# Performance work log

Hardware: AMD Instinct MI355X
Metric: run time of the kernel (lower is better)

## Reference

```python
import jax, jax.numpy as jnp
import numpy as np

P = 32    # cardinality (number of parallel paths)
C = 256   # block input/output channels
D = 4     # bottleneck width per path
EPS = 1e-3  # Keras BatchNormalization default epsilon


def setup_inputs() -> dict:
    key = jax.random.key(0)
    ks = jax.random.split(key, 24)
    def nrm(k, shape, s=0.05):
        return jax.random.normal(k, shape, dtype=jnp.float32) * s
    inp = {}
    inp["x"] = jax.random.normal(ks[0], (8, 56, 56, C), dtype=jnp.float32)
    # conv weights/biases, stacked over the path axis P
    inp["W1"] = nrm(ks[1], (P, C, D))          # 1x1 conv C->4
    inp["B1"] = nrm(ks[2], (P, D))
    inp["W2"] = nrm(ks[3], (P, 3, 3, D, D))    # 3x3 conv 4->4 (HWIO)
    inp["B2"] = nrm(ks[4], (P, D))
    inp["W3"] = nrm(ks[5], (P, D, C))          # 1x1 conv 4->256
    inp["B3"] = nrm(ks[6], (P, C))
    # BatchNorm (inference): gamma, beta, moving mean, moving var per stage
    inp["G1"]  = 1.0 + nrm(ks[7], (P, D));  inp["Be1"] = nrm(ks[8], (P, D))
    inp["M1"]  = nrm(ks[9], (P, D));        inp["V1"]  = 1.0 + 0.1 * jax.random.uniform(ks[10], (P, D), dtype=jnp.float32)
    inp["G2"]  = 1.0 + nrm(ks[11], (P, D)); inp["Be2"] = nrm(ks[12], (P, D))
    inp["M2"]  = nrm(ks[13], (P, D));       inp["V2"]  = 1.0 + 0.1 * jax.random.uniform(ks[14], (P, D), dtype=jnp.float32)
    inp["G3"]  = 1.0 + nrm(ks[15], (P, C)); inp["Be3"] = nrm(ks[16], (P, C))
    inp["M3"]  = nrm(ks[17], (P, C));       inp["V3"]  = 1.0 + 0.1 * jax.random.uniform(ks[18], (P, C), dtype=jnp.float32)
    return inp


def _bn(x, g, b, m, v):
    # inference batch-norm: affine over channel axis
    return g * (x - m) * jax.lax.rsqrt(v + EPS) + b


def _path(x, w1, b1, g1, be1, m1, v1, w2, b2, g2, be2, m2, v2, w3, b3, g3, be3, m3, v3):
    h = jnp.einsum('nhwc,cd->nhwd', x, w1) + b1            # 1x1 conv C->D
    h = jax.nn.relu(_bn(h, g1, be1, m1, v1))
    h = jax.lax.conv_general_dilated(
        h, w2, window_strides=(1, 1), padding='SAME',
        dimension_numbers=('NHWC', 'HWIO', 'NHWC')) + b2   # 3x3 conv D->D
    h = jax.nn.relu(_bn(h, g2, be2, m2, v2))
    h = jnp.einsum('nhwd,dc->nhwc', h, w3) + b3            # 1x1 conv D->C
    h = jax.nn.relu(_bn(h, g3, be3, m3, v3))
    return h  # Dropout(0.2) is identity at inference


def reference(x, W1, B1, G1, Be1, M1, V1, W2, B2, G2, Be2, M2, V2, W3, B3, G3, Be3, M3, V3):
    # vmap over the 32 cardinality paths; x is shared (in_axes=None)
    paths = jax.vmap(_path, in_axes=(None,) + (0,) * 18)(
        x, W1, B1, G1, Be1, M1, V1, W2, B2, G2, Be2, M2, V2, W3, B3, G3, Be3, M3, V3)
    return jax.nn.relu(paths.sum(axis=0) + x)
```

## Files before the change

### kernel.cpp

```cpp
#include <hip/hip_runtime.h>

#define BATCH 8
#define HH 56
#define WW 56
#define NPOS (BATCH*HH*WW)
#define C 256
#define P 32
#define D 4
#define J 128
#define EPS 1e-3f

typedef __attribute__((ext_vector_type(8))) short bf16x8_t;
typedef __attribute__((ext_vector_type(4))) float f32x4_t;

__device__ __forceinline__ unsigned short f2bf(float f) {
    union { float f; unsigned int i; } v; v.f = f;
    unsigned int r = v.i + 0x7fffu + ((v.i >> 16) & 1u);
    return (unsigned short)(r >> 16);
}
__device__ __forceinline__ uint2 pack4_trunc(float4 v) {
    uint2 r;
    r.x = __builtin_amdgcn_perm(__float_as_uint(v.y), __float_as_uint(v.x), 0x07060302u);
    r.y = __builtin_amdgcn_perm(__float_as_uint(v.w), __float_as_uint(v.z), 0x07060302u);
    return r;
}

__global__ __launch_bounds__(256) void fold_params(
    const float* __restrict__ W1, const float* __restrict__ B1,
    const float* __restrict__ W2, const float* __restrict__ B2,
    const float* __restrict__ W3, const float* __restrict__ B3,
    const float* __restrict__ G1, const float* __restrict__ Be1,
    const float* __restrict__ M1, const float* __restrict__ V1,
    const float* __restrict__ G2, const float* __restrict__ Be2,
    const float* __restrict__ M2, const float* __restrict__ V2,
    const float* __restrict__ G3, const float* __restrict__ Be3,
    const float* __restrict__ M3, const float* __restrict__ V3,
    unsigned short* __restrict__ W1bf, float* __restrict__ b1f,
    float* __restrict__ w2q, float* __restrict__ b2t,
    unsigned short* __restrict__ WB)
{
    int idx = blockIdx.x * 256 + threadIdx.x;

    if (idx < C*J) {
        int j = idx >> 8, c = idx & 255;
        int p = j >> 2, d = j & 3;
        float s = G1[j] * rsqrtf(V1[j] + EPS);
        W1bf[idx] = f2bf(W1[(p*C + c)*D + d] * s);
        return;
    }
    idx -= C*J;
    if (idx < J) {
        float s = G1[idx] * rsqrtf(V1[idx] + EPS);
        b1f[idx] = B1[idx] * s + Be1[idx] - M1[idx] * s;
        return;
    }
    idx -= J;
    if (idx < 9*D*D*P) {
        int do_ = idx & 3, p = (idx >> 2) & 31;
        int r2 = idx >> 7, di = r2 & 3, k9 = r2 >> 2;
        int j = p*4 + do_;
        float s = G2[j] * rsqrtf(V2[j] + EPS);
        w2q[idx] = W2[((p*9 + k9)*4 + di)*4 + do_] * s;
        return;
    }
    idx -= 9*D*D*P;
    if (idx < J) {
        int do_ = idx >> 5, p = idx & 31;
        int j = p*4 + do_;
        float s = G2[j] * rsqrtf(V2[j] + EPS);
        b2t[idx] = B2[j] * s + Be2[j] - M2[j] * s;
        return;
    }
    idx -= J;
    if (idx < P*C*8) {
        int s8 = idx & 7;
        int c = (idx >> 3) & 255;
        int p = idx >> 11;
        float sc = G3[p*C + c] * rsqrtf(V3[p*C + c] + EPS);
        float v = 0.f;
        if (s8 < 4)       v = W3[(p*D + s8)*C + c] * sc;
        else if (s8 == 4) v = B3[p*C + c] * sc + Be3[p*C + c] - M3[p*C + c] * sc;
        WB[idx] = f2bf(v);
        return;
    }
}

__global__ __launch_bounds__(256) void fused12(
    const float* __restrict__ x, const unsigned short* __restrict__ W1bf,
    const float* __restrict__ b1f, const float* __restrict__ w2q,
    const float* __restrict__ b2t, unsigned short* __restrict__ h2)
{
    __shared__ unsigned short xs[64*256];
    __shared__ unsigned short h1L[64*132];
    __shared__ float w2s[4608];
    __shared__ float bs[128];
    __shared__ float b1s[128];

    const int tid = threadIdx.x;
    int bxx = blockIdx.x;
    const int xb = bxx % 7;  bxx /= 7;
    const int yb = bxx % 14; const int b = bxx / 14;
    const int wid = tid >> 6, l = tid & 63, l15 = l & 15, quad = l >> 4;
    const int j0w = wid * 32;

    union bu { uint4 u; bf16x8_t v; };
    bu aw[2][8];
#pragma unroll
    for (int jf = 0; jf < 2; ++jf) {
        int row = j0w + jf*16 + l15;
#pragma unroll
        for (int kc = 0; kc < 8; ++kc)
            aw[jf][kc].u = *(const uint4*)&W1bf[row*C + kc*32 + quad*8];
    }

    for (int i = tid; i < 4608; i += 256) w2s[i] = w2q[i];
    if (tid < 128) { bs[tid] = b2t[tid]; b1s[tid] = b1f[tid]; }

#pragma unroll
    for (int it = 0; it < 8; ++it) {
        int idx = it*256 + tid;
        int pos = idx >> 5, g = idx & 31;
        uint4 st; st.x = 0u; st.y = 0u; st.z = 0u; st.w = 0u;
        if (pos < 60) {
            int hy = pos / 10, hx = pos - hy*10;
            int gy = yb*4 + hy - 1, gx = xb*8 + hx - 1;
            if (gy >= 0 && gy < HH && gx >= 0 && gx < WW) {
                const float* xp = &x[(size_t)((b*HH + gy)*WW + gx) * C + g*8];
                float4 v0 = *(const float4*)xp;
                float4 v1 = *(const float4*)(xp + 4);
                uint2 p0 = pack4_trunc(v0), p1 = pack4_trunc(v1);
                st.x = p0.x; st.y = p0.y; st.z = p1.x; st.w = p1.y;
            }
        }
        *(uint4*)&xs[pos*256 + ((g ^ (pos & 7)) * 8)] = st;
    }
    __syncthreads();

#pragma unroll
    for (int mt = 0; mt < 4; ++mt) {
        const int row = mt*16 + l15;
        int hy = (row * 205) >> 11;
        int hx = row - hy*10;
        int gy = yb*4 + hy - 1, gx = xb*8 + hx - 1;
        unsigned mask = (row < 60 && gy >= 0 && gy < HH && gx >= 0 && gx < WW)
                        ? 0xFFFFFFFFu : 0u;
        f32x4_t acc0 = (f32x4_t){0.f,0.f,0.f,0.f};
        f32x4_t acc1 = (f32x4_t){0.f,0.f,0.f,0.f};
#pragma unroll
        for (int kc = 0; kc < 8; ++kc) {
            int g = (kc*4 + quad) ^ (row & 7);
            bf16x8_t bb = *(const bf16x8_t*)&xs[row*256 + g*8];
            acc0 = __builtin_amdgcn_mfma_f32_16x16x32_bf16(aw[0][kc].v, bb, acc0, 0, 0, 0);
            acc1 = __builtin_amdgcn_mfma_f32_16x16x32_bf16(aw[1][kc].v, bb, acc1, 0, 0, 0);
        }
#pragma unroll
        for (int jf = 0; jf < 2; ++jf) {
            const f32x4_t a = jf ? acc1 : acc0;
            int jb = j0w + jf*16 + quad*4;
            float4 bias = *(const float4*)&b1s[jb];
            float v0 = fmaxf(a[0] + bias.x, 0.f);
            float v1 = fmaxf(a[1] + bias.y, 0.f);
            float v2 = fmaxf(a[2] + bias.z, 0.f);
            float v3 = fmaxf(a[3] + bias.w, 0.f);
            uint2 o;
            o.x = ((unsigned int)f2bf(v0) | ((unsigned int)f2bf(v1) << 16)) & mask;
            o.y = ((unsigned int)f2bf(v2) | ((unsigned int)f2bf(v3) << 16)) & mask;
            *(uint2*)&h1L[row*132 + jb] = o;
        }
    }
    __syncthreads();

    const int p = tid & 31;
    const int slot = tid >> 5;
    float acc[4][4];
#pragma unroll
    for (int i = 0; i < 4; ++i) {
        acc[i][0] = bs[p]; acc[i][1] = bs[32+p];
        acc[i][2] = bs[64+p]; acc[i][3] = bs[96+p];
    }
#pragma unroll
    for (int ky = 0; ky < 3; ++ky) {
#pragma unroll
        for (int kx = 0; kx < 3; ++kx) {
            const float* wp = &w2s[(ky*3 + kx) * 512 + p*4];
            float4 w0 = *(const float4*)&wp[0];
            float4 w1 = *(const float4*)&wp[128];
            float4 w2v = *(const float4*)&wp[256];
            float4 w3v = *(const float4*)&wp[384];
#pragma unroll
            for (int i = 0; i < 4; ++i) {
                int nl = slot + i*8;
                int hp = ((nl >> 3) + ky)*10 + (nl & 7) + kx;
                uint2 hv = *(const uint2*)&h1L[hp*132 + p*4];
                float f0 = __uint_as_float(hv.x << 16);
                float f1 = __uint_as_float(hv.x & 0xffff0000u);
                float f2 = __uint_as_float(hv.y << 16);
                float f3 = __uint_as_float(hv.y & 0xffff0000u);
                acc[i][0] = fmaf(f0, w0.x, acc[i][0]);  acc[i][1] = fmaf(f0, w0.y, acc[i][1]);
                acc[i][2] = fmaf(f0, w0.z, acc[i][2]);  acc[i][3] = fmaf(f0, w0.w, acc[i][3]);
                acc[i][0] = fmaf(f1, w1.x, acc[i][0]);  acc[i][1] = fmaf(f1, w1.y, acc[i][1]);
                acc[i][2] = fmaf(f1, w1.z, acc[i][2]);  acc[i][3] = fmaf(f1, w1.w, acc[i][3]);
                acc[i][0] = fmaf(f2, w2v.x, acc[i][0]); acc[i][1] = fmaf(f2, w2v.y, acc[i][1]);
                acc[i][2] = fmaf(f2, w2v.z, acc[i][2]); acc[i][3] = fmaf(f2, w2v.w, acc[i][3]);
                acc[i][0] = fmaf(f3, w3v.x, acc[i][0]); acc[i][1] = fmaf(f3, w3v.y, acc[i][1]);
                acc[i][2] = fmaf(f3, w3v.z, acc[i][2]); acc[i][3] = fmaf(f3, w3v.w, acc[i][3]);
            }
        }
    }
#pragma unroll
    for (int i = 0; i < 4; ++i) {
        int nl = slot + i*8;
        int gy = yb*4 + (nl >> 3), gx = xb*8 + (nl & 7);
        uint2 o;
        o.x = (unsigned int)f2bf(fmaxf(acc[i][0], 0.f)) |
              ((unsigned int)f2bf(fmaxf(acc[i][1], 0.f)) << 16);
        o.y = (unsigned int)f2bf(fmaxf(acc[i][2], 0.f)) |
              ((unsigned int)f2bf(fmaxf(acc[i][3], 0.f)) << 16);
        int n = (b*HH + gy)*WW + gx;
        *(uint2*)&h2[(size_t)n * J + p*4] = o;
    }
}

#define S3_STRIDE 136
__global__ __launch_bounds__(256, 3) void stage3(
    const unsigned short* __restrict__ h2,
    const unsigned short* __restrict__ WB,
    const float* __restrict__ x, float* __restrict__ out)
{
    __shared__ unsigned short h2s[64 * S3_STRIDE];
    __shared__ unsigned short wbf[P * 64 * 8];
    __shared__ unsigned short zz[8];

    const int tid = threadIdx.x;
    const int bx = blockIdx.x;
    const int cchunk = bx & 3, nchunk = bx >> 2;
    const int wid = tid >> 6, l = tid & 63, l15 = l & 15, quad = l >> 4;
    const int cb = cchunk * 64;
    const int cl = wid*16 + l15;
    const int c = cb + cl;
    const int n0 = nchunk * 64;

#pragma unroll
    for (int it = 0; it < 4; ++it) {
        int idx = it*256 + tid;
        int row = idx >> 4, col = (idx & 15) * 8;
        uint4 v = *(const uint4*)&h2[(size_t)(n0 + row) * J + col];
        *(uint4*)&h2s[row * S3_STRIDE + col] = v;
    }
#pragma unroll
    for (int it = 0; it < 8; ++it) {
        int e = it*256 + tid;
        int p = e >> 6, ecl = e & 63;
        uint4 u = *(const uint4*)&WB[((size_t)(p*C + cb + ecl)) * 8];
        *(uint4*)&wbf[(p*64 + ecl) * 8] = u;
    }
    if (tid < 8) zz[tid] = 0;
    __syncthreads();

    const unsigned short* bp = (quad == 0) ? &wbf[cl*8] : &zz[0];
    const int pstep = (quad == 0) ? 512 : 0;

    const f32x4_t zero = (f32x4_t){0.f, 0.f, 0.f, 0.f};
    f32x4_t acc[4];
#pragma unroll
    for (int i = 0; i < 4; ++i) acc[i] = zero;
    const unsigned int one = 0x3f80u;

#pragma unroll
    for (int p = 0; p < P; p += 2) {
        union { uint4 u; bf16x8_t v; } B0, B1;
        B0.u = *(const uint4*)(bp + p*pstep);
        B1.u = *(const uint4*)(bp + (p+1)*pstep);
#pragma unroll
        for (int pass = 0; pass < 4; ++pass) {
            uint4 h8 = *(const uint4*)&h2s[(pass*16 + l15) * S3_STRIDE + p*4];
            union { unsigned int u[4]; bf16x8_t v; } A0, A1;
            A0.u[0] = h8.x; A0.u[1] = h8.y; A0.u[2] = one; A0.u[3] = 0u;
            A1.u[0] = h8.z; A1.u[1] = h8.w; A1.u[2] = one; A1.u[3] = 0u;
            f32x4_t z0 = __builtin_amdgcn_mfma_f32_16x16x32_bf16(A0.v, B0.v, zero, 0, 0, 0);
            f32x4_t z1 = __builtin_amdgcn_mfma_f32_16x16x32_bf16(A1.v, B1.v, zero, 0, 0, 0);
#pragma unroll
            for (int r = 0; r < 4; ++r)
                acc[pass][r] += fmaxf(z0[r], 0.f) + fmaxf(z1[r], 0.f);
        }
    }

#pragma unroll
    for (int pass = 0; pass < 4; ++pass) {
#pragma unroll
        for (int r = 0; r < 4; ++r) {
            int n = n0 + pass*16 + quad*4 + r;
            float v = acc[pass][r] + x[(size_t)n * C + c];
            out[(size_t)n * C + c] = fmaxf(v, 0.f);
        }
    }
}

extern "C" void kernel_launch(void* const* d_in, const int* in_sizes, int n_in,
                              void* d_out, int out_size, void* d_ws, size_t ws_size,
                              hipStream_t stream) {
    const float* x  = (const float*)d_in[0];
    const float* W1 = (const float*)d_in[1];
    const float* B1 = (const float*)d_in[2];
    const float* W2 = (const float*)d_in[3];
    const float* B2 = (const float*)d_in[4];
    const float* W3 = (const float*)d_in[5];
    const float* B3 = (const float*)d_in[6];
    const float* G1 = (const float*)d_in[7];
    const float* Be1= (const float*)d_in[8];
    const float* M1 = (const float*)d_in[9];
    const float* V1 = (const float*)d_in[10];
    const float* G2 = (const float*)d_in[11];
    const float* Be2= (const float*)d_in[12];
    const float* M2 = (const float*)d_in[13];
    const float* V2 = (const float*)d_in[14];
    const float* G3 = (const float*)d_in[15];
    const float* Be3= (const float*)d_in[16];
    const float* M3 = (const float*)d_in[17];
    const float* V3 = (const float*)d_in[18];

    char* wsb = (char*)d_ws;
    unsigned short* h2   = (unsigned short*)(wsb + 0);
    unsigned short* W1bf = (unsigned short*)(wsb + 6422528);
    unsigned short* WB   = (unsigned short*)(wsb + 6488064);
    float*          w2q  = (float*)(wsb + 6619136);
    float*          b1f  = (float*)(wsb + 6637568);
    float*          b2t  = (float*)(wsb + 6638080);

    const int fold_tasks = C*J + J + 9*D*D*P + J + P*C*8;
    fold_params<<<(fold_tasks + 255)/256, 256, 0, stream>>>(
        W1, B1, W2, B2, W3, B3, G1, Be1, M1, V1, G2, Be2, M2, V2,
        G3, Be3, M3, V3, W1bf, b1f, w2q, b2t, WB);

    fused12<<<8*14*7, 256, 0, stream>>>(x, W1bf, b1f, w2q, b2t, h2);
    stage3<<<(NPOS/64)*4, 256, 0, stream>>>(h2, WB, x, (float*)d_out);
}
```

Measured before the change: 160.1 us.

## Fuse stage3 expansion into fused12 kernel, keeping h2 tile in shared memory

```diff
diff --git a/kernel.cpp b/kernel.cpp
--- a/kernel.cpp
+++ b/kernel.cpp
@@ -9,6 +9,7 @@
 #define D 4
 #define J 128
 #define EPS 1e-3f
+#define H2S 136
 
 typedef __attribute__((ext_vector_type(8))) short bf16x8_t;
 typedef __attribute__((ext_vector_type(4))) float f32x4_t;
@@ -37,7 +38,7 @@
     const float* __restrict__ M3, const float* __restrict__ V3,
     unsigned short* __restrict__ W1bf, float* __restrict__ b1f,
     float* __restrict__ w2q, float* __restrict__ b2t,
-    unsigned short* __restrict__ WB)
+    unsigned short* __restrict__ WB, unsigned short* __restrict__ zb)
 {
     int idx = blockIdx.x * 256 + threadIdx.x;
 
@@ -83,18 +84,22 @@
         WB[idx] = f2bf(v);
         return;
     }
-}
-
-__global__ __launch_bounds__(256) void fused12(
+    idx -= P*C*8;
+    if (idx < 8) { zb[idx] = 0; return; }
+}
+
+__global__ __launch_bounds__(256) void fused_all(
     const float* __restrict__ x, const unsigned short* __restrict__ W1bf,
     const float* __restrict__ b1f, const float* __restrict__ w2q,
-    const float* __restrict__ b2t, unsigned short* __restrict__ h2)
+    const float* __restrict__ b2t, const unsigned short* __restrict__ WB,
+    const unsigned short* __restrict__ zb, float* __restrict__ out)
 {
     __shared__ unsigned short xs[64*256];
     __shared__ unsigned short h1L[64*132];
     __shared__ float w2s[4608];
     __shared__ float bs[128];
     __shared__ float b1s[128];
+    __shared__ unsigned short h2s[32*H2S];
 
     const int tid = threadIdx.x;
     int bxx = blockIdx.x;
@@ -210,88 +215,78 @@
 #pragma unroll
     for (int i = 0; i < 4; ++i) {
         int nl = slot + i*8;
-        int gy = yb*4 + (nl >> 3), gx = xb*8 + (nl & 7);
         uint2 o;
         o.x = (unsigned int)f2bf(fmaxf(acc[i][0], 0.f)) |
               ((unsigned int)f2bf(fmaxf(acc[i][1], 0.f)) << 16);
         o.y = (unsigned int)f2bf(fmaxf(acc[i][2], 0.f)) |
               ((unsigned int)f2bf(fmaxf(acc[i][3], 0.f)) << 16);
-        int n = (b*HH + gy)*WW + gx;
-        *(uint2*)&h2[(size_t)n * J + p*4] = o;
-    }
-}
-
-#define S3_STRIDE 136
-__global__ __launch_bounds__(256, 3) void stage3(
-    const unsigned short* __restrict__ h2,
-    const unsigned short* __restrict__ WB,
-    const float* __restrict__ x, float* __restrict__ out)
-{
-    __shared__ unsigned short h2s[64 * S3_STRIDE];
-    __shared__ unsigned short wbf[P * 64 * 8];
-    __shared__ unsigned short zz[8];
-
-    const int tid = threadIdx.x;
-    const int bx = blockIdx.x;
-    const int cchunk = bx & 3, nchunk = bx >> 2;
-    const int wid = tid >> 6, l = tid & 63, l15 = l & 15, quad = l >> 4;
-    const int cb = cchunk * 64;
-    const int cl = wid*16 + l15;
-    const int c = cb + cl;
-    const int n0 = nchunk * 64;
-
-#pragma unroll
-    for (int it = 0; it < 4; ++it) {
-        int idx = it*256 + tid;
-        int row = idx >> 4, col = (idx & 15) * 8;
-        uint4 v = *(const uint4*)&h2[(size_t)(n0 + row) * J + col];
-        *(uint4*)&h2s[row * S3_STRIDE + col] = v;
-    }
-#pragma unroll
-    for (int it = 0; it < 8; ++it) {
-        int e = it*256 + tid;
-        int p = e >> 6, ecl = e & 63;
-        uint4 u = *(const uint4*)&WB[((size_t)(p*C + cb + ecl)) * 8];
-        *(uint4*)&wbf[(p*64 + ecl) * 8] = u;
-    }
-    if (tid < 8) zz[tid] = 0;
+        *(uint2*)&h2s[nl*H2S + p*4] = o;
+    }
     __syncthreads();
 
-    const unsigned short* bp = (quad == 0) ? &wbf[cl*8] : &zz[0];
-    const int pstep = (quad == 0) ? 512 : 0;
+    const int cb = wid * 64;
+    const unsigned short* wbp;
+    int pstr, cstr;
+    if (quad == 0) {
+        wbp = &WB[((size_t)(cb + l15)) * 8];
+        pstr = C * 8;
+        cstr = 16 * 8;
+    } else {
+        wbp = zb;
+        pstr = 0; cstr = 0;
+    }
 
     const f32x4_t zero = (f32x4_t){0.f, 0.f, 0.f, 0.f};
-    f32x4_t acc[4];
-#pragma unroll
-    for (int i = 0; i < 4; ++i) acc[i] = zero;
+    f32x4_t dacc[2][4];
+#pragma unroll
+    for (int ps = 0; ps < 2; ++ps)
+#pragma unroll
+        for (int ct = 0; ct < 4; ++ct) dacc[ps][ct] = zero;
     const unsigned int one = 0x3f80u;
 
-#pragma unroll
-    for (int p = 0; p < P; p += 2) {
-        union { uint4 u; bf16x8_t v; } B0, B1;
-        B0.u = *(const uint4*)(bp + p*pstep);
-        B1.u = *(const uint4*)(bp + (p+1)*pstep);
-#pragma unroll
-        for (int pass = 0; pass < 4; ++pass) {
-            uint4 h8 = *(const uint4*)&h2s[(pass*16 + l15) * S3_STRIDE + p*4];
-            union { unsigned int u[4]; bf16x8_t v; } A0, A1;
-            A0.u[0] = h8.x; A0.u[1] = h8.y; A0.u[2] = one; A0.u[3] = 0u;
-            A1.u[0] = h8.z; A1.u[1] = h8.w; A1.u[2] = one; A1.u[3] = 0u;
-            f32x4_t z0 = __builtin_amdgcn_mfma_f32_16x16x32_bf16(A0.v, B0.v, zero, 0, 0, 0);
-            f32x4_t z1 = __builtin_amdgcn_mfma_f32_16x16x32_bf16(A1.v, B1.v, zero, 0, 0, 0);
-#pragma unroll
-            for (int r = 0; r < 4; ++r)
-                acc[pass][r] += fmaxf(z0[r], 0.f) + fmaxf(z1[r], 0.f);
-        }
-    }
-
-#pragma unroll
-    for (int pass = 0; pass < 4; ++pass) {
+#pragma unroll 2
+    for (int pp = 0; pp < 16; ++pp) {
+        uint4 h0 = *(const uint4*)&h2s[l15*H2S + pp*8];
+        uint4 h1 = *(const uint4*)&h2s[(16 + l15)*H2S + pp*8];
+        union au { unsigned int u[4]; bf16x8_t v; };
+        au A00, A01, A10, A11;
+        A00.u[0] = h0.x; A00.u[1] = h0.y; A00.u[2] = one; A00.u[3] = 0u;
+        A01.u[0] = h0.z; A01.u[1] = h0.w; A01.u[2] = one; A01.u[3] = 0u;
+        A10.u[0] = h1.x; A10.u[1] = h1.y; A10.u[2] = one; A10.u[3] = 0u;
+        A11.u[0] = h1.z; A11.u[1] = h1.w; A11.u[2] = one; A11.u[3] = 0u;
+        const unsigned short* pb0 = wbp + pp*2*pstr;
+        const unsigned short* pb1 = pb0 + pstr;
+#pragma unroll
+        for (int ct = 0; ct < 4; ++ct) {
+            union bu2 { uint4 u; bf16x8_t v; } B0, B1;
+            B0.u = *(const uint4*)(pb0 + ct*cstr);
+            B1.u = *(const uint4*)(pb1 + ct*cstr);
+            f32x4_t z00 = __builtin_amdgcn_mfma_f32_16x16x32_bf16(A00.v, B0.v, zero, 0, 0, 0);
+            f32x4_t z01 = __builtin_amdgcn_mfma_f32_16x16x32_bf16(A01.v, B1.v, zero, 0, 0, 0);
+            f32x4_t z10 = __builtin_amdgcn_mfma_f32_16x16x32_bf16(A10.v, B0.v, zero, 0, 0, 0);
+            f32x4_t z11 = __builtin_amdgcn_mfma_f32_16x16x32_bf16(A11.v, B1.v, zero, 0, 0, 0);
+#pragma unroll
+            for (int r = 0; r < 4; ++r) {
+                dacc[0][ct][r] += fmaxf(z00[r], 0.f) + fmaxf(z01[r], 0.f);
+                dacc[1][ct][r] += fmaxf(z10[r], 0.f) + fmaxf(z11[r], 0.f);
+            }
+        }
+    }
+
+#pragma unroll
+    for (int ps = 0; ps < 2; ++ps) {
 #pragma unroll
         for (int r = 0; r < 4; ++r) {
-            int n = n0 + pass*16 + quad*4 + r;
-            float v = acc[pass][r] + x[(size_t)n * C + c];
-            out[(size_t)n * C + c] = fmaxf(v, 0.f);
+            int nl = ps*16 + quad*4 + r;
+            int gy = yb*4 + (nl >> 3), gx = xb*8 + (nl & 7);
+            size_t n = (size_t)((b*HH + gy)*WW + gx);
+            const float* xr = &x[n*C + cb + l15];
+            float* orow = &out[n*C + cb + l15];
+#pragma unroll
+            for (int ct = 0; ct < 4; ++ct) {
+                float v = dacc[ps][ct][r] + xr[ct*16];
+                orow[ct*16] = fmaxf(v, 0.f);
+            }
         }
     }
 }
@@ -320,18 +315,18 @@
     const float* V3 = (const float*)d_in[18];
 
     char* wsb = (char*)d_ws;
-    unsigned short* h2   = (unsigned short*)(wsb + 0);
-    unsigned short* W1bf = (unsigned short*)(wsb + 6422528);
-    unsigned short* WB   = (unsigned short*)(wsb + 6488064);
-    float*          w2q  = (float*)(wsb + 6619136);
-    float*          b1f  = (float*)(wsb + 6637568);
-    float*          b2t  = (float*)(wsb + 6638080);
-
-    const int fold_tasks = C*J + J + 9*D*D*P + J + P*C*8;
+    unsigned short* W1bf = (unsigned short*)(wsb + 0);
+    unsigned short* WB   = (unsigned short*)(wsb + 65536);
+    float*          w2q  = (float*)(wsb + 196608);
+    float*          b1f  = (float*)(wsb + 215040);
+    float*          b2t  = (float*)(wsb + 215552);
+    unsigned short* zb   = (unsigned short*)(wsb + 216064);
+
+    const int fold_tasks = C*J + J + 9*D*D*P + J + P*C*8 + 8;
     fold_params<<<(fold_tasks + 255)/256, 256, 0, stream>>>(
         W1, B1, W2, B2, W3, B3, G1, Be1, M1, V1, G2, Be2, M2, V2,
-        G3, Be3, M3, V3, W1bf, b1f, w2q, b2t, WB);
-
-    fused12<<<8*14*7, 256, 0, stream>>>(x, W1bf, b1f, w2q, b2t, h2);
-    stage3<<<(NPOS/64)*4, 256, 0, stream>>>(h2, WB, x, (float*)d_out);
-}
+        G3, Be3, M3, V3, W1bf, b1f, w2q, b2t, WB, zb);
+
+    fused_all<<<8*14*7, 256, 0, stream>>>(x, W1bf, b1f, w2q, b2t, WB, zb,
+                                          (float*)d_out);
+}
```

New measurement: 180.5 us. +12.8%, slower.
